# Kernel tuning notes

Hardware: AMD Instinct MI355X
Metric: run time of the kernel (lower is better)

The kernel has to match this reference:

```python
import jax, jax.numpy as jnp
import numpy as np

USER = 100000
ITEM = 100000
N = USER + ITEM          # total nodes
D = 64                   # latdim
DEG = 16                 # avg edges per user (before symmetrization)
L_GNN = 2                # args.gnn_layer
L_MLP = 2                # args.layer_mlp
EPS = 1e-5               # LayerNorm eps


def setup_inputs() -> dict:
    key = jax.random.key(0)
    k1, k2, k3, k4, k5 = jax.random.split(key, 5)
    # bipartite user->item edges, then symmetrize (bi_adj over N x N nodes)
    u = jax.random.randint(k1, (USER * DEG,), 0, USER)
    v = jax.random.randint(k2, (USER * DEG,), 0, ITEM) + USER
    rows = jnp.concatenate([u, v]).astype(jnp.int64)
    cols = jnp.concatenate([v, u]).astype(jnp.int64)
    # symmetric D^-1/2 A D^-1/2 normalization (matches _normalize_adj)
    deg = jnp.zeros((N,), jnp.float32).at[rows].add(1.0)
    vals = 1.0 / (jnp.sqrt(deg[rows]) * jnp.sqrt(deg[cols]))
    # xavier-uniform-ish initial embeddings (detached in the source)
    bound = float(np.sqrt(6.0 / (N + D)))
    ini_embeds = jax.random.uniform(k3, (N, D), jnp.float32, -bound, bound)
    # MLP params: L_MLP stacked Linear(latdim, latdim)
    wb = float(np.sqrt(6.0 / (D + D)))
    Ws = jax.random.uniform(k4, (L_MLP, D, D), jnp.float32, -wb, wb)
    bs = jnp.zeros((L_MLP, D), jnp.float32)
    gamma = jnp.ones((D,), jnp.float32)
    beta = jnp.zeros((D,), jnp.float32)
    return {"rows": rows, "cols": cols, "vals": vals, "ini_embeds": ini_embeds,
            "Ws": Ws, "bs": bs, "gamma": gamma, "beta": beta}


def reference(rows, cols, vals, ini_embeds, Ws, bs, gamma, beta):
    # UntrainedGCN.forward: multi-hop spmm propagation (concat=0, symetric=True)
    e = ini_embeds
    for _ in range(L_GNN):
        # spmm: out[r] += vals * e[c] for each edge (r, c)
        e = jax.ops.segment_sum(vals[:, None] * e[cols], rows, num_segments=N)
    # residual MLP: relu(Wx+b) + x per FeedForwardLayer
    for i in range(L_MLP):
        e = jax.nn.relu(e @ Ws[i].T + bs[i]) + e
    # LayerNorm over last dim
    mu = e.mean(-1, keepdims=True)
    xc = e - mu
    var = (xc * xc).mean(-1, keepdims=True)
    e = xc * jax.lax.rsqrt(var + EPS) * gamma + beta
    return e[:USER], e[USER:]
```

## Files before the change

kernel.cpp:

```cpp
#include <hip/hip_runtime.h>
#include <hip/hip_bf16.h>

#define NN      200000
#define D       64
#define NTILE   12500
#define BKT_SH  8
#define BKT_RW  256
#define NBKT    782
#define L2CAP   7680
#define CPAD    16
#define RSENT   256

typedef __attribute__((ext_vector_type(8))) short short8;
typedef __attribute__((ext_vector_type(4))) short short4v;
typedef __attribute__((ext_vector_type(4))) float f32x4;

__device__ inline unsigned short f32_to_bf16_rne(float x) {
    unsigned u = __float_as_uint(x);
    unsigned r = u + 0x7FFFu + ((u >> 16) & 1u);
    return (unsigned short)(r >> 16);
}
__device__ inline float bf16_bits_to_f32(unsigned short h) {
    return __uint_as_float(((unsigned)h) << 16);
}
__device__ inline unsigned pack2_bf16_rne(float lo, float hi) {
    unsigned a = __float_as_uint(lo);
    unsigned b = __float_as_uint(hi);
    a = a + 0x7FFFu + ((a >> 16) & 1u);
    b = b + 0x7FFFu + ((b >> 16) & 1u);
    return (a >> 16) | (b & 0xFFFF0000u);
}
__device__ inline float bf_lo(unsigned u) { return __uint_as_float(u << 16); }
__device__ inline float bf_hi(unsigned u) { return __uint_as_float(u & 0xFFFF0000u); }

__global__ __launch_bounds__(256) void zero_f4(float4* __restrict__ p, int n4) {
    int i = blockIdx.x * blockDim.x + threadIdx.x;
    if (i < n4) p[i] = make_float4(0.f, 0.f, 0.f, 0.f);
}
__global__ __launch_bounds__(256) void zero_i(int* __restrict__ p, int n) {
    int i = blockIdx.x * blockDim.x + threadIdx.x;
    if (i < n) p[i] = 0;
}
__global__ __launch_bounds__(256) void cvt_bf16(const float2* __restrict__ in,
                                                unsigned* __restrict__ out, int n) {
    int stride = gridDim.x * blockDim.x;
    for (int i = blockIdx.x * blockDim.x + threadIdx.x; i < n; i += stride) {
        float2 v = in[i];
        out[i] = pack2_bf16_rne(v.x, v.y);
    }
}

template <int ALIGN>
__global__ __launch_bounds__(1024) void bkt_count(const int* __restrict__ rows,
                                                  int* __restrict__ tot_p,
                                                  int E, int epb) {
    __shared__ int h[NBKT];
    int t = threadIdx.x;
    for (int i = t; i < NBKT; i += 1024) h[i] = 0;
    __syncthreads();
    int start = blockIdx.x * epb;
    int end   = min(E, start + epb);
    for (int e = start + t; e < end; e += 1024)
        atomicAdd(&h[rows[e] >> BKT_SH], 1);
    __syncthreads();
    for (int i = t; i < NBKT; i += 1024) {
        int c   = h[i];
        int res = (c + ALIGN - 1) & ~(ALIGN - 1);
        if (res) atomicAdd(&tot_p[i * CPAD], res);
    }
}

__global__ __launch_bounds__(1024) void bkt_scan(const int* __restrict__ tot_p,
                                                 int* __restrict__ bktstart,
                                                 int* __restrict__ cursor_p) {
    __shared__ int s[1024];
    int t = threadIdx.x;
    int v = (t < NBKT) ? tot_p[t * CPAD] : 0;
    s[t] = v;
    __syncthreads();
    #pragma unroll
    for (int d = 1; d < 1024; d <<= 1) {
        int a = (t >= d) ? s[t - d] : 0;
        __syncthreads();
        s[t] += a;
        __syncthreads();
    }
    if (t < NBKT) {
        int ex = s[t] - v;
        bktstart[t] = ex;
        cursor_p[t * CPAD] = ex;
    }
    if (t == 0) bktstart[NBKT] = s[1023];
}

template <int ALIGN>
__global__ __launch_bounds__(1024) void scatter_l1(const int* __restrict__ rows,
                                                   const int* __restrict__ cols,
                                                   const float* __restrict__ vals,
                                                   int* __restrict__ cursor_p,
                                                   int2* __restrict__ packed,
                                                   int E, int epb) {
    __shared__ int h[NBKT];
    __shared__ int base[NBKT];
    int t = threadIdx.x;
    for (int i = t; i < NBKT; i += 1024) h[i] = 0;
    __syncthreads();
    int start = blockIdx.x * epb;
    int end   = min(E, start + epb);
    for (int e = start + t; e < end; e += 1024)
        atomicAdd(&h[rows[e] >> BKT_SH], 1);
    __syncthreads();
    for (int i = t; i < NBKT; i += 1024) {
        int c   = h[i];
        int res = (c + ALIGN - 1) & ~(ALIGN - 1);
        int b0  = res ? atomicAdd(&cursor_p[i * CPAD], res) : 0;
        base[i] = b0;
        for (int j = c; j < res; ++j)
            packed[b0 + j] = make_int2(RSENT << 18, 0);
        h[i] = 0;
    }
    __syncthreads();
    for (int e = start + t; e < end; e += 1024) {
        int r = rows[e];
        int b = r >> BKT_SH;
        int p = base[b] + atomicAdd(&h[b], 1);
        packed[p] = make_int2(cols[e] | ((r & (BKT_RW - 1)) << 18),
                              __float_as_int(vals[e]));
    }
}

__global__ __launch_bounds__(256) void sort_l2(const int* __restrict__ bktstart,
                                               int2* __restrict__ packed,
                                               int* __restrict__ rp,
                                               int* __restrict__ rpe) {
    __shared__ int2 sm[L2CAP];
    __shared__ int  cnt[BKT_RW];
    __shared__ int  cur[BKT_RW];
    int b = blockIdx.x;
    int s = bktstart[b];
    int e = bktstart[b + 1];
    int n = e - s;
    if (n > L2CAP) n = L2CAP;
    int t = threadIdx.x;
    cnt[t] = 0;
    __syncthreads();
    for (int i = t; i < n; i += 256) {
        int2 v = packed[s + i];
        sm[i] = v;
        int r = (v.x >> 18) & 0x1FF;
        if (r < BKT_RW) atomicAdd(&cnt[r], 1);
    }
    __syncthreads();
    #pragma unroll
    for (int d = 1; d < BKT_RW; d <<= 1) {
        int a = (t >= d) ? cnt[t - d] : 0;
        __syncthreads();
        cnt[t] += a;
        __syncthreads();
    }
    {
        int ex = t ? cnt[t - 1] : 0;
        cur[t] = ex;
        int g = (b << BKT_SH) + t;
        if (g < NN) { rp[g] = s + ex; rpe[g] = s + cnt[t]; }
    }
    __syncthreads();
    for (int i = t; i < n; i += 256) {
        int2 v = sm[i];
        int  r = (v.x >> 18) & 0x1FF;
        if (r < BKT_RW) {
            int p = atomicAdd(&cur[r], 1);
            packed[s + p] = make_int2(v.x & 0x3FFFF, v.y);
        }
    }
}

__global__ __launch_bounds__(256) void spmm_g(const int* __restrict__ rp,
                                              const int* __restrict__ rpe,
                                              const int2* __restrict__ packed,
                                              const uint2* __restrict__ ein,
                                              uint2* __restrict__ out_bf, int n) {
    int wave = (blockIdx.x * 256 + threadIdx.x) >> 6;
    int lane = threadIdx.x & 63;
    int l    = lane & 15;
    int row  = wave * 4 + (lane >> 4);
    if (row >= n) return;

    float ax = 0.f, ay = 0.f, az = 0.f, aw = 0.f;
    int s = rp[row], e = rpe[row];
    for (int base = s; base < e; base += 16) {
        int cnt = e - base; if (cnt > 16) cnt = 16;
        int2 ev = make_int2(0, 0);
        if (l < cnt) ev = packed[base + l];
        int k = 0;
        for (; k + 4 <= cnt; k += 4) {
            int   c0 = __shfl(ev.x, k,     16), c1 = __shfl(ev.x, k + 1, 16);
            int   c2 = __shfl(ev.x, k + 2, 16), c3 = __shfl(ev.x, k + 3, 16);
            float v0 = __int_as_float(__shfl(ev.y, k,     16));
            float v1 = __int_as_float(__shfl(ev.y, k + 1, 16));
            float v2 = __int_as_float(__shfl(ev.y, k + 2, 16));
            float v3 = __int_as_float(__shfl(ev.y, k + 3, 16));
            uint2 g0 = ein[c0 * 16 + l];
            uint2 g1 = ein[c1 * 16 + l];
            uint2 g2 = ein[c2 * 16 + l];
            uint2 g3 = ein[c3 * 16 + l];
            ax += v0 * bf_lo(g0.x); ay += v0 * bf_hi(g0.x);
            az += v0 * bf_lo(g0.y); aw += v0 * bf_hi(g0.y);
            ax += v1 * bf_lo(g1.x); ay += v1 * bf_hi(g1.x);
            az += v1 * bf_lo(g1.y); aw += v1 * bf_hi(g1.y);
            ax += v2 * bf_lo(g2.x); ay += v2 * bf_hi(g2.x);
            az += v2 * bf_lo(g2.y); aw += v2 * bf_hi(g2.y);
            ax += v3 * bf_lo(g3.x); ay += v3 * bf_hi(g3.x);
            az += v3 * bf_lo(g3.y); aw += v3 * bf_hi(g3.y);
        }
        for (; k < cnt; ++k) {
            int   c0 = __shfl(ev.x, k, 16);
            float v0 = __int_as_float(__shfl(ev.y, k, 16));
            uint2 g0 = ein[c0 * 16 + l];
            ax += v0 * bf_lo(g0.x); ay += v0 * bf_hi(g0.x);
            az += v0 * bf_lo(g0.y); aw += v0 * bf_hi(g0.y);
        }
    }
    out_bf[(size_t)row * 16 + l] = make_uint2(pack2_bf16_rne(ax, ay), pack2_bf16_rne(az, aw));
}

__global__ __launch_bounds__(256) void spmm_scatter(const int* __restrict__ rows,
                                                    const int* __restrict__ cols,
                                                    const float* __restrict__ vals,
                                                    const float* __restrict__ ein,
                                                    float* __restrict__ eout, int E) {
    int gid  = blockIdx.x * blockDim.x + threadIdx.x;
    int wid  = gid >> 6;
    int lane = threadIdx.x & 63;
    int nw   = (gridDim.x * blockDim.x) >> 6;
    for (int e = wid; e < E; e += nw) {
        int   r = rows[e];
        int   c = cols[e];
        float v = vals[e];
        float x = ein[(size_t)c * D + lane];
        unsafeAtomicAdd(&eout[(size_t)r * D + lane], v * x);
    }
}

template <int IN_BF16>
__global__ __launch_bounds__(256) void mlp_v2(const uint2* __restrict__ in_bf,
                                              float* __restrict__ out,
                                              const float* __restrict__ Ws,
                                              const float* __restrict__ bs,
                                              const float* __restrict__ gamma,
                                              const float* __restrict__ beta) {
    __shared__ unsigned short wlds[2][64][72];
    __shared__ float tb[4][16][68];

    int t    = threadIdx.x;
    int wv   = t >> 6;
    int lane = t & 63;
    int fr   = t & 15;
    int fq   = lane >> 4;

    for (int i = t * 4; i < 2 * 64 * 64; i += 1024) {
        float4 f = *(const float4*)(Ws + i);
        int l = i >> 12, r = (i >> 6) & 63, c = i & 63;
        short4v s4;
        s4[0] = (short)f32_to_bf16_rne(f.x);
        s4[1] = (short)f32_to_bf16_rne(f.y);
        s4[2] = (short)f32_to_bf16_rne(f.z);
        s4[3] = (short)f32_to_bf16_rne(f.w);
        *(short4v*)&wlds[l][r][c] = s4;
    }
    __syncthreads();

    float bia[2][4], gam[4], bet[4];
    #pragma unroll
    for (int nt = 0; nt < 4; ++nt) {
        bia[0][nt] = bs[nt * 16 + fr];
        bia[1][nt] = bs[64 + nt * 16 + fr];
        gam[nt]    = gamma[nt * 16 + fr];
        bet[nt]    = beta[nt * 16 + fr];
    }

    float (*tw)[68] = tb[wv];

    for (int tile = blockIdx.x * 4 + wv; tile < NTILE; tile += gridDim.x * 4) {
        float* baseo = out + (size_t)tile * 1024;

        if (IN_BF16) {
            const uint2* bi = in_bf + (size_t)tile * 256;
            #pragma unroll
            for (int it = 0; it < 4; ++it) {
                int idx = it * 64 + lane;
                uint2 u = bi[idx];
                int r = idx >> 4, c = (idx & 15) * 4;
                tw[r][c]     = bf_lo(u.x);
                tw[r][c + 1] = bf_hi(u.x);
                tw[r][c + 2] = bf_lo(u.y);
                tw[r][c + 3] = bf_hi(u.y);
            }
        } else {
            #pragma unroll
            for (int it = 0; it < 4; ++it) {
                int idx = it * 256 + lane * 4;
                *(float4*)&tw[idx >> 6][idx & 63] = *(const float4*)(baseo + idx);
            }
        }

        #pragma unroll
        for (int l = 0; l < 2; ++l) {
            short8 xh[2], xl[2];
            #pragma unroll
            for (int kk = 0; kk < 2; ++kk) {
                const float* s = &tw[fr][kk * 32 + fq * 8];
                float4 a = *(const float4*)s;
                float4 b4 = *(const float4*)(s + 4);
                float v[8] = {a.x, a.y, a.z, a.w, b4.x, b4.y, b4.z, b4.w};
                #pragma unroll
                for (int j = 0; j < 8; ++j) {
                    unsigned short hh = f32_to_bf16_rne(v[j]);
                    xh[kk][j] = (short)hh;
                    xl[kk][j] = (short)f32_to_bf16_rne(v[j] - bf16_bits_to_f32(hh));
                }
            }
            f32x4 acc[4];
            #pragma unroll
            for (int nt = 0; nt < 4; ++nt) {
                float bb = bia[l][nt];
                acc[nt] = f32x4{bb, bb, bb, bb};
                #pragma unroll
                for (int kk = 0; kk < 2; ++kk) {
                    short8 w8 = *(const short8*)&wlds[l][nt * 16 + fr][kk * 32 + fq * 8];
                    if (!(IN_BF16 && l == 0))
                        acc[nt] = __builtin_amdgcn_mfma_f32_16x16x32_bf16(xl[kk], w8, acc[nt], 0, 0, 0);
                    acc[nt] = __builtin_amdgcn_mfma_f32_16x16x32_bf16(xh[kk], w8, acc[nt], 0, 0, 0);
                }
            }
            #pragma unroll
            for (int nt = 0; nt < 4; ++nt)
                #pragma unroll
                for (int j = 0; j < 4; ++j) {
                    float* cell = &tw[fq * 4 + j][nt * 16 + fr];
                    *cell = fmaxf(acc[nt][j], 0.f) + *cell;
                }
        }

        float y2[4][4], sm[4], sq[4];
        #pragma unroll
        for (int j = 0; j < 4; ++j) { sm[j] = 0.f; sq[j] = 0.f; }
        #pragma unroll
        for (int nt = 0; nt < 4; ++nt)
            #pragma unroll
            for (int j = 0; j < 4; ++j) {
                float v = tw[fq * 4 + j][nt * 16 + fr];
                y2[nt][j] = v;
                sm[j] += v; sq[j] += v * v;
            }
        #pragma unroll
        for (int off = 1; off < 16; off <<= 1) {
            #pragma unroll
            for (int j = 0; j < 4; ++j) {
                sm[j] += __shfl_xor(sm[j], off);
                sq[j] += __shfl_xor(sq[j], off);
            }
        }
        #pragma unroll
        for (int j = 0; j < 4; ++j) {
            float mu  = sm[j] * (1.f / 64.f);
            float var = sq[j] * (1.f / 64.f) - mu * mu;
            float rs  = rsqrtf(var + 1e-5f);
            #pragma unroll
            for (int nt = 0; nt < 4; ++nt)
                tw[fq * 4 + j][nt * 16 + fr] = (y2[nt][j] - mu) * rs * gam[nt] + bet[nt];
        }

        #pragma unroll
        for (int it = 0; it < 4; ++it) {
            int idx = it * 256 + lane * 4;
            *(float4*)(baseo + idx) = *(const float4*)&tw[idx >> 6][idx & 63];
        }
    }
}

template <int ALIGN>
static void run_csr(const int* rows, const int* cols, const float* vals,
                    const float* ini, float* out, char* w, int E, size_t packed_cap,
                    int nchunk, const float* Ws, const float* bs,
                    const float* gamma, const float* beta, hipStream_t stream) {
    size_t inibf_b  = (size_t)NN * 32 * 4;
    size_t e1bf_b   = inibf_b;
    size_t packed_b = packed_cap * 8;
    size_t rp_b     = (((size_t)NN + 1) * 4 + 63) & ~(size_t)63;
    size_t rpe_b    = (ALIGN > 1) ? rp_b : 0;
    size_t bsrt_b   = (((size_t)NBKT + 1) * 4 + 63) & ~(size_t)63;
    size_t pad_b    = (size_t)NBKT * CPAD * 4;

    unsigned* ini_bf   = (unsigned*)w;  w += inibf_b;
    unsigned* e1_bf    = (unsigned*)w;  w += e1bf_b;
    int2*     packed   = (int2*)w;      w += packed_b;
    int*      rp       = (int*)w;       w += rp_b;
    int*      rpe      = (ALIGN > 1) ? (int*)w : rp + 1;  w += rpe_b;
    int*      bktstart = (int*)w;       w += bsrt_b;
    int*      tot_p    = (int*)w;       w += pad_b;
    int*      cursor_p = (int*)w;

    int epb = (E + nchunk - 1) / nchunk;
    cvt_bf16<<<2048, 256, 0, stream>>>((const float2*)ini, ini_bf, NN * 32);
    zero_i<<<(NBKT * CPAD + 255) / 256, 256, 0, stream>>>(tot_p, NBKT * CPAD);
    bkt_count<ALIGN><<<nchunk, 1024, 0, stream>>>(rows, tot_p, E, epb);
    bkt_scan<<<1, 1024, 0, stream>>>(tot_p, bktstart, cursor_p);
    scatter_l1<ALIGN><<<nchunk, 1024, 0, stream>>>(rows, cols, vals, cursor_p, packed, E, epb);
    sort_l2<<<NBKT, 256, 0, stream>>>(bktstart, packed, rp, rpe);

    spmm_g<<<NTILE, 256, 0, stream>>>(rp, rpe, packed, (const uint2*)ini_bf,
                                      (uint2*)e1_bf, NN);
    spmm_g<<<NTILE, 256, 0, stream>>>(rp, rpe, packed, (const uint2*)e1_bf,
                                      (uint2*)ini_bf, NN);
    mlp_v2<1><<<1024, 256, 0, stream>>>((const uint2*)ini_bf, out, Ws, bs, gamma, beta);
}

extern "C" void kernel_launch(void* const* d_in, const int* in_sizes, int n_in,
                              void* d_out, int out_size, void* d_ws, size_t ws_size,
                              hipStream_t stream) {
    const int*   rows  = (const int*)d_in[0];
    const int*   cols  = (const int*)d_in[1];
    const float* vals  = (const float*)d_in[2];
    const float* ini   = (const float*)d_in[3];
    const float* Ws    = (const float*)d_in[4];
    const float* bs    = (const float*)d_in[5];
    const float* gamma = (const float*)d_in[6];
    const float* beta  = (const float*)d_in[7];
    float* out = (float*)d_out;
    int E = in_sizes[0];

    size_t inibf_b = (size_t)NN * 32 * 4;
    size_t rp_b    = (((size_t)NN + 1) * 4 + 63) & ~(size_t)63;
    size_t bsrt_b  = (((size_t)NBKT + 1) * 4 + 63) & ~(size_t)63;
    size_t pad_b   = (size_t)NBKT * CPAD * 4;
    auto cap  = [&](int nc) { return (size_t)E + (size_t)NBKT * nc * 7; };
    auto need = [&](int nc, int nrp) {
        return 2 * inibf_b + cap(nc) * 8 + (size_t)nrp * rp_b + bsrt_b + 2 * pad_b;
    };

    if (ws_size >= need(512, 2)) {
        run_csr<8>(rows, cols, vals, ini, out, (char*)d_ws, E, cap(512), 512,
                   Ws, bs, gamma, beta, stream);
    } else if (ws_size >= need(256, 2)) {
        run_csr<8>(rows, cols, vals, ini, out, (char*)d_ws, E, cap(256), 256,
                   Ws, bs, gamma, beta, stream);
    } else if (ws_size >= 2 * inibf_b + (size_t)E * 8 + rp_b + bsrt_b + 2 * pad_b) {
        run_csr<1>(rows, cols, vals, ini, out, (char*)d_ws, E, (size_t)E, 256,
                   Ws, bs, gamma, beta, stream);
    } else {
        float* e1 = (float*)d_ws;
        int n4 = out_size / 4;
        int zb = (n4 + 255) / 256;
        zero_f4<<<zb, 256, 0, stream>>>((float4*)e1,  n4);
        zero_f4<<<zb, 256, 0, stream>>>((float4*)out, n4);
        spmm_scatter<<<12800, 256, 0, stream>>>(rows, cols, vals, ini, e1, E);
        spmm_scatter<<<12800, 256, 0, stream>>>(rows, cols, vals, e1, out, E);
        mlp_v2<0><<<1024, 256, 0, stream>>>(nullptr, out, Ws, bs, gamma, beta);
    }
}
```

Baseline: 243.7 us.

## Build CSR in one scatter pass using per-block runs instead of count+scatter

Merges the separate bucket-count and scatter kernels into one pass. Each block scans its local bucket histogram, reserves a contiguous region with a single global atomic, writes edges there and records a (start,len) run per bucket. The second-level sort then gathers each bucket's runs via binary search into shared memory and writes the final row-sorted CSR to a separate buffer, dropping alignment padding, sentinel entries and the rpe array. This saves one full read of rows and a kernel launch, at the cost of an extra edge buffer, a run list, and binary-search gathers in the sort.

```diff
diff --git a/kernel.cpp b/kernel.cpp
--- a/kernel.cpp
+++ b/kernel.cpp
@@ -7,9 +7,10 @@
 #define BKT_SH  8
 #define BKT_RW  256
 #define NBKT    782
-#define L2CAP   7680
+#define NCH     512
+#define MAXRUN  512
+#define SCAP    4864
 #define CPAD    16
-#define RSENT   256
 
 typedef __attribute__((ext_vector_type(8))) short short8;
 typedef __attribute__((ext_vector_type(4))) short short4v;
@@ -50,11 +51,19 @@
     }
 }
 
-template <int ALIGN>
-__global__ __launch_bounds__(1024) void bkt_count(const int* __restrict__ rows,
-                                                  int* __restrict__ tot_p,
-                                                  int E, int epb) {
+__global__ __launch_bounds__(1024) void scatter_v3(const int* __restrict__ rows,
+                                                   const int* __restrict__ cols,
+                                                   const float* __restrict__ vals,
+                                                   int* __restrict__ gcur,
+                                                   int* __restrict__ runcnt_p,
+                                                   int2* __restrict__ runlist,
+                                                   int* __restrict__ tot_p,
+                                                   int2* __restrict__ packed1,
+                                                   int E, int epb) {
     __shared__ int h[NBKT];
+    __shared__ int off[NBKT];
+    __shared__ int s[1024];
+    __shared__ int gbase;
     int t = threadIdx.x;
     for (int i = t; i < NBKT; i += 1024) h[i] = 0;
     __syncthreads();
@@ -63,16 +72,42 @@
     for (int e = start + t; e < end; e += 1024)
         atomicAdd(&h[rows[e] >> BKT_SH], 1);
     __syncthreads();
+    int v = (t < NBKT) ? h[t] : 0;
+    s[t] = v;
+    __syncthreads();
+    #pragma unroll
+    for (int d = 1; d < 1024; d <<= 1) {
+        int a = (t >= d) ? s[t - d] : 0;
+        __syncthreads();
+        s[t] += a;
+        __syncthreads();
+    }
+    if (t < NBKT) off[t] = s[t] - v;
+    if (t == 1023) gbase = atomicAdd(gcur, s[1023]);
+    __syncthreads();
+    int gb = gbase;
     for (int i = t; i < NBKT; i += 1024) {
-        int c   = h[i];
-        int res = (c + ALIGN - 1) & ~(ALIGN - 1);
-        if (res) atomicAdd(&tot_p[i * CPAD], res);
-    }
-}
-
-__global__ __launch_bounds__(1024) void bkt_scan(const int* __restrict__ tot_p,
-                                                 int* __restrict__ bktstart,
-                                                 int* __restrict__ cursor_p) {
+        int c = h[i];
+        if (c) {
+            int idx = atomicAdd(&runcnt_p[i * CPAD], 1);
+            runlist[(size_t)i * MAXRUN + idx] = make_int2(gb + off[i], c);
+            atomicAdd(&tot_p[i * CPAD], c);
+        }
+        h[i] = 0;
+    }
+    __syncthreads();
+    for (int e = start + t; e < end; e += 1024) {
+        int r = rows[e];
+        int b = r >> BKT_SH;
+        int p = gb + off[b] + atomicAdd(&h[b], 1);
+        packed1[p] = make_int2(cols[e] | ((r & (BKT_RW - 1)) << 18),
+                               __float_as_int(vals[e]));
+    }
+}
+
+__global__ __launch_bounds__(1024) void bkt_scan3(const int* __restrict__ tot_p,
+                                                  int* __restrict__ bktstart,
+                                                  int* __restrict__ rp, int E) {
     __shared__ int s[1024];
     int t = threadIdx.x;
     int v = (t < NBKT) ? tot_p[t * CPAD] : 0;
@@ -85,93 +120,72 @@
         s[t] += a;
         __syncthreads();
     }
-    if (t < NBKT) {
-        int ex = s[t] - v;
-        bktstart[t] = ex;
-        cursor_p[t * CPAD] = ex;
-    }
-    if (t == 0) bktstart[NBKT] = s[1023];
-}
-
-template <int ALIGN>
-__global__ __launch_bounds__(1024) void scatter_l1(const int* __restrict__ rows,
-                                                   const int* __restrict__ cols,
-                                                   const float* __restrict__ vals,
-                                                   int* __restrict__ cursor_p,
-                                                   int2* __restrict__ packed,
-                                                   int E, int epb) {
-    __shared__ int h[NBKT];
-    __shared__ int base[NBKT];
-    int t = threadIdx.x;
-    for (int i = t; i < NBKT; i += 1024) h[i] = 0;
-    __syncthreads();
-    int start = blockIdx.x * epb;
-    int end   = min(E, start + epb);
-    for (int e = start + t; e < end; e += 1024)
-        atomicAdd(&h[rows[e] >> BKT_SH], 1);
-    __syncthreads();
-    for (int i = t; i < NBKT; i += 1024) {
-        int c   = h[i];
-        int res = (c + ALIGN - 1) & ~(ALIGN - 1);
-        int b0  = res ? atomicAdd(&cursor_p[i * CPAD], res) : 0;
-        base[i] = b0;
-        for (int j = c; j < res; ++j)
-            packed[b0 + j] = make_int2(RSENT << 18, 0);
-        h[i] = 0;
-    }
-    __syncthreads();
-    for (int e = start + t; e < end; e += 1024) {
-        int r = rows[e];
-        int b = r >> BKT_SH;
-        int p = base[b] + atomicAdd(&h[b], 1);
-        packed[p] = make_int2(cols[e] | ((r & (BKT_RW - 1)) << 18),
-                              __float_as_int(vals[e]));
-    }
-}
-
-__global__ __launch_bounds__(256) void sort_l2(const int* __restrict__ bktstart,
-                                               int2* __restrict__ packed,
-                                               int* __restrict__ rp,
-                                               int* __restrict__ rpe) {
-    __shared__ int2 sm[L2CAP];
+    if (t < NBKT) bktstart[t] = s[t] - v;
+    if (t == 0) { bktstart[NBKT] = E; rp[NN] = E; }
+}
+
+__global__ __launch_bounds__(512) void sort_v3(const int* __restrict__ bktstart,
+                                               const int* __restrict__ runcnt_p,
+                                               const int2* __restrict__ runlist,
+                                               const int2* __restrict__ packed1,
+                                               int2* __restrict__ packed2,
+                                               int* __restrict__ rp) {
+    __shared__ int2 sm[SCAP];
+    __shared__ int  runoff[MAXRUN];
+    __shared__ int  rstart[MAXRUN];
+    __shared__ int  s2[512];
     __shared__ int  cnt[BKT_RW];
     __shared__ int  cur[BKT_RW];
+    __shared__ int  nsh;
     int b = blockIdx.x;
-    int s = bktstart[b];
-    int e = bktstart[b + 1];
-    int n = e - s;
-    if (n > L2CAP) n = L2CAP;
     int t = threadIdx.x;
-    cnt[t] = 0;
-    __syncthreads();
-    for (int i = t; i < n; i += 256) {
-        int2 v = packed[s + i];
+    int rc = runcnt_p[b * CPAD];
+
+    int len = 0, st = 0;
+    if (t < rc) { int2 rl = runlist[(size_t)b * MAXRUN + t]; st = rl.x; len = rl.y; }
+    rstart[t] = st;
+    s2[t] = len;
+    __syncthreads();
+    #pragma unroll
+    for (int d = 1; d < 512; d <<= 1) {
+        int a = (t >= d) ? s2[t - d] : 0;
+        __syncthreads();
+        s2[t] += a;
+        __syncthreads();
+    }
+    runoff[t] = s2[t] - len;
+    if (t == 511) nsh = s2[511];
+    if (t < BKT_RW) cnt[t] = 0;
+    __syncthreads();
+    int n = nsh; if (n > SCAP) n = SCAP;
+
+    for (int i = t; i < n; i += 512) {
+        int lo = 0, hi = rc - 1;
+        while (lo < hi) { int mid = (lo + hi + 1) >> 1; if (runoff[mid] <= i) lo = mid; else hi = mid - 1; }
+        int2 v = packed1[rstart[lo] + (i - runoff[lo])];
         sm[i] = v;
-        int r = (v.x >> 18) & 0x1FF;
-        if (r < BKT_RW) atomicAdd(&cnt[r], 1);
+        atomicAdd(&cnt[(v.x >> 18) & (BKT_RW - 1)], 1);
     }
     __syncthreads();
     #pragma unroll
     for (int d = 1; d < BKT_RW; d <<= 1) {
-        int a = (t >= d) ? cnt[t - d] : 0;
-        __syncthreads();
-        cnt[t] += a;
-        __syncthreads();
-    }
-    {
+        int a = (t >= d && t < BKT_RW) ? cnt[t - d] : 0;
+        __syncthreads();
+        if (t < BKT_RW) cnt[t] += a;
+        __syncthreads();
+    }
+    int sgl = bktstart[b];
+    if (t < BKT_RW) {
         int ex = t ? cnt[t - 1] : 0;
         cur[t] = ex;
         int g = (b << BKT_SH) + t;
-        if (g < NN) { rp[g] = s + ex; rpe[g] = s + cnt[t]; }
-    }
-    __syncthreads();
-    for (int i = t; i < n; i += 256) {
+        if (g < NN) rp[g] = sgl + ex;
+    }
+    __syncthreads();
+    for (int i = t; i < n; i += 512) {
         int2 v = sm[i];
-        int  r = (v.x >> 18) & 0x1FF;
-        if (r < BKT_RW) {
-            int p = atomicAdd(&cur[r], 1);
-            packed[s + p] = make_int2(v.x & 0x3FFFF, v.y);
-        }
+        int  p = atomicAdd(&cur[(v.x >> 18) & (BKT_RW - 1)], 1);
+        packed2[sgl + p] = make_int2(v.x & 0x3FFFF, v.y);
     }
 }
 
@@ -379,43 +393,6 @@
     }
 }
 
-template <int ALIGN>
-static void run_csr(const int* rows, const int* cols, const float* vals,
-                    const float* ini, float* out, char* w, int E, size_t packed_cap,
-                    int nchunk, const float* Ws, const float* bs,
-                    const float* gamma, const float* beta, hipStream_t stream) {
-    size_t inibf_b  = (size_t)NN * 32 * 4;
-    size_t e1bf_b   = inibf_b;
-    size_t packed_b = packed_cap * 8;
-    size_t rp_b     = (((size_t)NN + 1) * 4 + 63) & ~(size_t)63;
-    size_t rpe_b    = (ALIGN > 1) ? rp_b : 0;
-    size_t bsrt_b   = (((size_t)NBKT + 1) * 4 + 63) & ~(size_t)63;
-    size_t pad_b    = (size_t)NBKT * CPAD * 4;
-
-    unsigned* ini_bf   = (unsigned*)w;  w += inibf_b;
-    unsigned* e1_bf    = (unsigned*)w;  w += e1bf_b;
-    int2*     packed   = (int2*)w;      w += packed_b;
-    int*      rp       = (int*)w;       w += rp_b;
-    int*      rpe      = (ALIGN > 1) ? (int*)w : rp + 1;  w += rpe_b;
-    int*      bktstart = (int*)w;       w += bsrt_b;
-    int*      tot_p    = (int*)w;       w += pad_b;
-    int*      cursor_p = (int*)w;
-
-    int epb = (E + nchunk - 1) / nchunk;
-    cvt_bf16<<<2048, 256, 0, stream>>>((const float2*)ini, ini_bf, NN * 32);
-    zero_i<<<(NBKT * CPAD + 255) / 256, 256, 0, stream>>>(tot_p, NBKT * CPAD);
-    bkt_count<ALIGN><<<nchunk, 1024, 0, stream>>>(rows, tot_p, E, epb);
-    bkt_scan<<<1, 1024, 0, stream>>>(tot_p, bktstart, cursor_p);
-    scatter_l1<ALIGN><<<nchunk, 1024, 0, stream>>>(rows, cols, vals, cursor_p, packed, E, epb);
-    sort_l2<<<NBKT, 256, 0, stream>>>(bktstart, packed, rp, rpe);
-
-    spmm_g<<<NTILE, 256, 0, stream>>>(rp, rpe, packed, (const uint2*)ini_bf,
-                                      (uint2*)e1_bf, NN);
-    spmm_g<<<NTILE, 256, 0, stream>>>(rp, rpe, packed, (const uint2*)e1_bf,
-                                      (uint2*)ini_bf, NN);
-    mlp_v2<1><<<1024, 256, 0, stream>>>((const uint2*)ini_bf, out, Ws, bs, gamma, beta);
-}
-
 extern "C" void kernel_launch(void* const* d_in, const int* in_sizes, int n_in,
                               void* d_out, int out_size, void* d_ws, size_t ws_size,
                               hipStream_t stream) {
@@ -430,24 +407,46 @@
     float* out = (float*)d_out;
     int E = in_sizes[0];
 
-    size_t inibf_b = (size_t)NN * 32 * 4;
-    size_t rp_b    = (((size_t)NN + 1) * 4 + 63) & ~(size_t)63;
-    size_t bsrt_b  = (((size_t)NBKT + 1) * 4 + 63) & ~(size_t)63;
-    size_t pad_b   = (size_t)NBKT * CPAD * 4;
-    auto cap  = [&](int nc) { return (size_t)E + (size_t)NBKT * nc * 7; };
-    auto need = [&](int nc, int nrp) {
-        return 2 * inibf_b + cap(nc) * 8 + (size_t)nrp * rp_b + bsrt_b + 2 * pad_b;
-    };
-
-    if (ws_size >= need(512, 2)) {
-        run_csr<8>(rows, cols, vals, ini, out, (char*)d_ws, E, cap(512), 512,
-                   Ws, bs, gamma, beta, stream);
-    } else if (ws_size >= need(256, 2)) {
-        run_csr<8>(rows, cols, vals, ini, out, (char*)d_ws, E, cap(256), 256,
-                   Ws, bs, gamma, beta, stream);
-    } else if (ws_size >= 2 * inibf_b + (size_t)E * 8 + rp_b + bsrt_b + 2 * pad_b) {
-        run_csr<1>(rows, cols, vals, ini, out, (char*)d_ws, E, (size_t)E, 256,
-                   Ws, bs, gamma, beta, stream);
+    size_t A_b   = (size_t)NN * 32 * 4;
+    size_t e8    = (size_t)E * 8;
+    size_t B_b   = (A_b > e8) ? A_b : e8;
+    size_t C_b   = e8;
+    size_t run_b = (size_t)NBKT * MAXRUN * 8;
+    size_t rcp_b = ((size_t)NBKT * CPAD * 4 + 63) & ~(size_t)63;
+    size_t gc_b  = 64;
+    size_t rp_b  = (((size_t)NN + 1) * 4 + 63) & ~(size_t)63;
+    size_t bst_b = (((size_t)NBKT + 1) * 4 + 63) & ~(size_t)63;
+    size_t need  = A_b + B_b + C_b + run_b + 2 * rcp_b + gc_b + rp_b + bst_b;
+
+    if (ws_size >= need) {
+        char* w = (char*)d_ws;
+        unsigned* Abuf     = (unsigned*)w;  w += A_b;
+        char*     Bbuf     = w;             w += B_b;
+        int2*     packed2  = (int2*)w;      w += C_b;
+        int2*     runlist  = (int2*)w;      w += run_b;
+        int*      runcnt_p = (int*)w;       w += rcp_b;
+        int*      tot_p    = (int*)w;       w += rcp_b;
+        int*      gcur     = (int*)w;       w += gc_b;
+        int*      rp       = (int*)w;       w += rp_b;
+        int*      bktstart = (int*)w;
+
+        int2*     packed1  = (int2*)Bbuf;
+        unsigned* e1_bf    = (unsigned*)Bbuf;
+
+        int epb = (E + NCH - 1) / NCH;
+        cvt_bf16<<<2048, 256, 0, stream>>>((const float2*)ini, Abuf, NN * 32);
+        int zn = (int)((2 * rcp_b + gc_b) / 4);
+        zero_i<<<(zn + 255) / 256, 256, 0, stream>>>(runcnt_p, zn);
+        scatter_v3<<<NCH, 1024, 0, stream>>>(rows, cols, vals, gcur, runcnt_p,
+                                             runlist, tot_p, packed1, E, epb);
+        bkt_scan3<<<1, 1024, 0, stream>>>(tot_p, bktstart, rp, E);
+        sort_v3<<<NBKT, 512, 0, stream>>>(bktstart, runcnt_p, runlist,
+                                          packed1, packed2, rp);
+        spmm_g<<<NTILE, 256, 0, stream>>>(rp, rp + 1, packed2, (const uint2*)Abuf,
+                                          (uint2*)e1_bf, NN);
+        spmm_g<<<NTILE, 256, 0, stream>>>(rp, rp + 1, packed2, (const uint2*)e1_bf,
+                                          (uint2*)Abuf, NN);
+        mlp_v2<1><<<1024, 256, 0, stream>>>((const uint2*)Abuf, out, Ws, bs, gamma, beta);
     } else {
         float* e1 = (float*)d_ws;
         int n4 = out_size / 4;
```

After: 248.7 us. 1.02x slower.
